# Performance work log

Measured on AMD Instinct MI355X. Metric: run time of the kernel, lower is better.

## Reference

```python
import jax, jax.numpy as jnp
import numpy as np

# Conv config (matches init_kwargs): 3x3 conv, 256->256, stride 1, pad 1
KH, KW = 3, 3
STRIDE = (1, 1)
PAD = ((1, 1), (1, 1))


def setup_inputs() -> dict:
    key = jax.random.key(0)
    k1, k2, k3 = jax.random.split(key, 3)
    x = jax.random.normal(k1, (32, 256, 56, 56), dtype=jnp.float32)
    # linear.weight = conv.weight.view(C_out, C_in*kH*kW) -> [256, 2304]
    weight = jax.random.normal(k2, (256, 256 * KH * KW), dtype=jnp.float32) * 0.02
    bias = jax.random.normal(k3, (256,), dtype=jnp.float32)
    return {"x": x, "weight": weight, "bias": bias}


def reference(x, weight, bias):
    # im2col (same layout/order as F.unfold: feature dim = C * kH * kW, c-major)
    # patches: [N, C*kH*kW, H_out, W_out]
    patches = jax.lax.conv_general_dilated_patches(
        x, filter_shape=(KH, KW), window_strides=STRIDE, padding=PAD
    )
    # dense GEMM over the unfolded feature dim (the nn.Linear)
    y = jnp.einsum("nkhw,ok->nohw", patches, weight)
    y = y + bias[None, :, None, None]
    return y
```

## Files before the change

kernel.cpp:

```cpp
#include <hip/hip_runtime.h>
#include <hip/hip_bf16.h>

typedef short bf16x8 __attribute__((ext_vector_type(8)));
typedef float f32x4  __attribute__((ext_vector_type(4)));

#define HWHW   3136
#define BH     4
#define NROW   6
#define NCOL   58
#define NJJ    (NROW*NCOL)
#define ROWSH  40
#define CHUNK  32
#define NCHUNK 8

__device__ __forceinline__ unsigned short f2bf(float f) {
    unsigned int u = __float_as_uint(f);
    u += 0x7fffu + ((u >> 16) & 1u);
    return (unsigned short)(u >> 16);
}

__global__ void wprep(const float* __restrict__ w, unsigned short* __restrict__ wt) {
    int idx = blockIdx.x * blockDim.x + threadIdx.x;
    int e    = idx & 7;
    int lane = (idx >> 3) & 63;
    int om   = (idx >> 9) & 15;
    int c8   = (idx >> 13) & 7;
    int t    = idx >> 16;
    int o = om * 16 + (lane & 15);
    int c = c8 * 32 + (lane >> 4) * 8 + e;
    wt[idx] = f2bf(w[o * 2304 + c * 9 + t]);
}

__global__ __launch_bounds__(512, 2)
void conv_kernel(const float* __restrict__ x, const unsigned short* __restrict__ wt,
                 const float* __restrict__ bias, float* __restrict__ out) {
    __shared__ short xs[2][NJJ * ROWSH];

    const int hb = blockIdx.x;
    const int n  = blockIdx.y;
    const int h0 = hb * BH;

    const int tid  = threadIdx.x;
    const int lane = tid & 63;
    const int wv   = tid >> 6;
    const int wm   = wv & 3;
    const int ng   = wv >> 2;
    const int g    = lane >> 4;
    const int lcol = lane & 15;

    int bbase[7];
#pragma unroll
    for (int f = 0; f < 7; ++f) {
        int j = ng * 112 + f * 16 + lcol;
        bbase[f] = ((j / 56) * NCOL + (j % 56)) * ROWSH + 8 * g;
    }

    const int cpair = tid >> 5;
    const int col0  = tid & 31;

    const float* xn = x + (size_t)n * 256 * HWHW;

    float sv0[6][2], sv1[6][2];

    f32x4 acc[4][7];
#pragma unroll
    for (int m = 0; m < 4; ++m)
#pragma unroll
        for (int f = 0; f < 7; ++f) acc[m][f] = (f32x4){0.f, 0.f, 0.f, 0.f};

    const unsigned short* wl = wt + (size_t)lane * 8;

    auto stage_load = [&](int c8) {
        const float* xc0 = xn + (size_t)(c8 * CHUNK + 2 * cpair) * HWHW;
        const float* xc1 = xc0 + HWHW;
#pragma unroll
        for (int r = 0; r < 6; ++r) {
            int hh = h0 - 1 + r;
            bool rok = (hh >= 0) & (hh < 56);
#pragma unroll
            for (int ci = 0; ci < 2; ++ci) {
                int col = col0 + 32 * ci;
                int ww  = col - 1;
                bool ok = rok & (col < 58) & (ww >= 0) & (ww < 56);
                int off = hh * 56 + ww;
                sv0[r][ci] = ok ? xc0[off] : 0.0f;
                sv1[r][ci] = ok ? xc1[off] : 0.0f;
            }
        }
    };
    auto stage_write = [&](int buf) {
#pragma unroll
        for (int r = 0; r < 6; ++r)
#pragma unroll
            for (int ci = 0; ci < 2; ++ci) {
                int col = col0 + 32 * ci;
                if (col < 58) {
                    unsigned int p = (unsigned int)f2bf(sv0[r][ci]) |
                                     ((unsigned int)f2bf(sv1[r][ci]) << 16);
                    *(unsigned int*)&xs[buf][(r * NCOL + col) * ROWSH + 2 * cpair] = p;
                }
            }
    };

    stage_load(0);
    stage_write(0);
    __syncthreads();

    for (int c8 = 0; c8 < NCHUNK; ++c8) {
        if (c8 < NCHUNK - 1) stage_load(c8 + 1);
        const short* xb = &xs[c8 & 1][0];

        bf16x8 a0[4], a1[4];
#pragma unroll
        for (int m = 0; m < 4; ++m)
            a0[m] = *(const bf16x8*)(wl + (size_t)(((0 * 8 + c8) * 16) + 4 * wm + m) * 512);

#pragma unroll
        for (int t = 0; t < 9; ++t) {
            bf16x8* ac = (t & 1) ? a1 : a0;
            bf16x8* an = (t & 1) ? a0 : a1;
            if (t < 8) {
#pragma unroll
                for (int m = 0; m < 4; ++m)
                    an[m] = *(const bf16x8*)(wl + (size_t)((((t + 1) * 8 + c8) * 16) + 4 * wm + m) * 512);
            }
            const int dt = ((t / 3) * NCOL + (t % 3)) * ROWSH;
#pragma unroll
            for (int f = 0; f < 7; ++f) {
                bf16x8 b = *(const bf16x8*)&xb[bbase[f] + dt];
#pragma unroll
                for (int m = 0; m < 4; ++m)
                    acc[m][f] = __builtin_amdgcn_mfma_f32_16x16x32_bf16(ac[m], b, acc[m][f], 0, 0, 0);
            }
        }

        if (c8 < NCHUNK - 1) stage_write((c8 + 1) & 1);
        __syncthreads();
    }

#pragma unroll
    for (int m = 0; m < 4; ++m) {
#pragma unroll
        for (int q = 0; q < 4; ++q) {
            int o = 64 * wm + 16 * m + 4 * g + q;
            float bs = bias[o];
            float* yo = out + ((size_t)n * 256 + o) * HWHW + h0 * 56;
#pragma unroll
            for (int f = 0; f < 7; ++f) {
                int j = ng * 112 + f * 16 + lcol;
                yo[j] = acc[m][f][q] + bs;
            }
        }
    }
}

extern "C" void kernel_launch(void* const* d_in, const int* in_sizes, int n_in,
                              void* d_out, int out_size, void* d_ws, size_t ws_size,
                              hipStream_t stream) {
    const float* x    = (const float*)d_in[0];
    const float* w    = (const float*)d_in[1];
    const float* bias = (const float*)d_in[2];
    float* out        = (float*)d_out;
    unsigned short* wt = (unsigned short*)d_ws;

    wprep<<<2304, 256, 0, stream>>>(w, wt);
    dim3 grid(14, 32);
    conv_kernel<<<grid, 512, 0, stream>>>(x, wt, bias, out);
}
```

Measured before the change: 128.2 us.

## Pre-pad input to bf16 buffer and split output channels across blocks

Adds an xprep kernel that converts the fp32 input into a zero-padded bf16 buffer of shape [N,C,58,64], so the conv kernel can fill shared memory with vector loads instead of bounds-checked scalar fp32 loads. The main conv kernel now runs 256-thread blocks, each covering half the output channels, which doubles the grid. The next chunk's stage loads and writes are interleaved partway through the tap loop, and weight loads are no longer double-buffered in registers. The cost is an extra kernel with a full read and write of the activation, and each input tile is now staged twice, once per channel half. The old kernel is kept as a fallback for when the workspace is too small.

After: 284.0 us. +121.6%, slower.

```diff
diff --git a/kernel.cpp b/kernel.cpp
--- a/kernel.cpp
+++ b/kernel.cpp
@@ -5,13 +5,10 @@
 typedef float f32x4  __attribute__((ext_vector_type(4)));
 
 #define HWHW   3136
-#define BH     4
-#define NROW   6
-#define NCOL   58
-#define NJJ    (NROW*NCOL)
-#define ROWSH  40
-#define CHUNK  32
-#define NCHUNK 8
+#define XP_H   58
+#define XP_W   64
+#define ROWSH  34
+#define NJJ    (6*64)
 
 __device__ __forceinline__ unsigned short f2bf(float f) {
     unsigned int u = __float_as_uint(f);
@@ -31,47 +28,155 @@
     wt[idx] = f2bf(w[o * 2304 + c * 9 + t]);
 }
 
-__global__ __launch_bounds__(512, 2)
-void conv_kernel(const float* __restrict__ x, const unsigned short* __restrict__ wt,
-                 const float* __restrict__ bias, float* __restrict__ out) {
+__global__ void xprep(const float* __restrict__ x, unsigned short* __restrict__ xp) {
+    int idx = blockIdx.x * 256 + threadIdx.x;
+    int n  = blockIdx.y;
+    int q  = idx & 15;
+    int t2 = idx >> 4;
+    int hp = t2 % 58;
+    int c  = t2 / 58;
+    int h_ok = (hp >= 1) & (hp <= 56);
+    const float* xr = x + ((size_t)n * 256 + c) * HWHW + (h_ok ? (hp - 1) : 0) * 56;
+    unsigned int v01 = 0, v23 = 0;
+#pragma unroll
+    for (int e = 0; e < 4; ++e) {
+        int w = q * 4 + e - 1;
+        bool ok = h_ok & (w >= 0) & (w < 56);
+        float f = xr[ok ? w : 0];
+        f = ok ? f : 0.0f;
+        unsigned int b = f2bf(f);
+        if (e < 2) v01 |= b << (16 * e);
+        else       v23 |= b << (16 * (e - 2));
+    }
+    unsigned int* dst = (unsigned int*)(xp + ((((size_t)n * 256 + c) * XP_H) + hp) * XP_W + q * 4);
+    dst[0] = v01;
+    dst[1] = v23;
+}
+
+__global__ __launch_bounds__(256, 2)
+void conv_main(const unsigned short* __restrict__ xp, const unsigned short* __restrict__ wt,
+               const float* __restrict__ bias, float* __restrict__ out) {
     __shared__ short xs[2][NJJ * ROWSH];
 
-    const int hb = blockIdx.x;
+    const int bx = blockIdx.x;
+    const int hb = bx >> 1;
+    const int bm = bx & 1;
     const int n  = blockIdx.y;
-    const int h0 = hb * BH;
+    const int h0 = hb * 4;
 
     const int tid  = threadIdx.x;
     const int lane = tid & 63;
     const int wv   = tid >> 6;
-    const int wm   = wv & 3;
-    const int ng   = wv >> 2;
+    const int wm   = wv & 1;
+    const int ng   = wv >> 1;
     const int g    = lane >> 4;
     const int lcol = lane & 15;
 
-    int bbase[7];
+    int bboff[7];
 #pragma unroll
     for (int f = 0; f < 7; ++f) {
         int j = ng * 112 + f * 16 + lcol;
-        bbase[f] = ((j / 56) * NCOL + (j % 56)) * ROWSH + 8 * g;
-    }
-
-    const int cpair = tid >> 5;
-    const int col0  = tid & 31;
-
+        bboff[f] = (((j / 56) * 64 + (j % 56)) * ROWSH + 8 * g) * 2;
+    }
+
+    const int so = tid & 7;
+    const int sc = (tid >> 3) & 31;
+    const unsigned short* xpt = xp + (((size_t)n * 256 + sc) * XP_H + h0) * XP_W + so * 8;
+    const int swb = ((so * 8) * ROWSH + sc) * 2;
+
+    const unsigned short* wl = wt + (size_t)lane * 8;
+    const int obase = bm * 8 + wm * 4;
+
+    f32x4 acc[4][7];
+#pragma unroll
+    for (int m = 0; m < 4; ++m)
+#pragma unroll
+        for (int f = 0; f < 7; ++f) acc[m][f] = (f32x4){0.f, 0.f, 0.f, 0.f};
+
+    bf16x8 sv[3];
+    auto s_load = [&](int c8, int half) {
+        const unsigned short* p = xpt + (size_t)c8 * 32 * XP_H * XP_W + half * 3 * XP_W;
+#pragma unroll
+        for (int r = 0; r < 3; ++r) sv[r] = *(const bf16x8*)(p + r * XP_W);
+    };
+    auto s_write = [&](int buf, int half) {
+        char* d = (char*)&xs[buf][0] + swb + half * 3 * 64 * ROWSH * 2;
+#pragma unroll
+        for (int r = 0; r < 3; ++r)
+#pragma unroll
+            for (int k = 0; k < 8; ++k)
+                *(short*)(d + r * 64 * ROWSH * 2 + k * ROWSH * 2) = sv[r][k];
+    };
+
+    s_load(0, 0); s_write(0, 0);
+    s_load(0, 1); s_write(0, 1);
+    __syncthreads();
+
+    for (int c8 = 0; c8 < 8; ++c8) {
+        const char* xb = (const char*)&xs[c8 & 1][0];
+        const bool more = c8 < 7;
+        if (more) s_load(c8 + 1, 0);
+
+#pragma unroll
+        for (int t = 0; t < 9; ++t) {
+            bf16x8 a[4];
+#pragma unroll
+            for (int m = 0; m < 4; ++m)
+                a[m] = *(const bf16x8*)(wl + (size_t)((t * 8 + c8) * 16 + obase + m) * 512);
+            const int dt = ((t / 3) * 64 + (t % 3)) * ROWSH * 2;
+#pragma unroll
+            for (int f = 0; f < 7; ++f) {
+                bf16x8 b = *(const bf16x8*)(xb + bboff[f] + dt);
+#pragma unroll
+                for (int m = 0; m < 4; ++m)
+                    acc[m][f] = __builtin_amdgcn_mfma_f32_16x16x32_bf16(a[m], b, acc[m][f], 0, 0, 0);
+            }
+            if (t == 2 && more) { s_write((c8 + 1) & 1, 0); s_load(c8 + 1, 1); }
+            if (t == 5 && more) { s_write((c8 + 1) & 1, 1); }
+        }
+        __syncthreads();
+    }
+
+#pragma unroll
+    for (int m = 0; m < 4; ++m) {
+#pragma unroll
+        for (int q = 0; q < 4; ++q) {
+            int o = bm * 128 + wm * 64 + m * 16 + 4 * g + q;
+            float bs = bias[o];
+            float* yo = out + ((size_t)n * 256 + o) * HWHW + hb * 224;
+#pragma unroll
+            for (int f = 0; f < 7; ++f) {
+                int j = ng * 112 + f * 16 + lcol;
+                yo[j] = acc[m][f][q] + bs;
+            }
+        }
+    }
+}
+
+__global__ __launch_bounds__(512, 2)
+void conv_fallback(const float* __restrict__ x, const unsigned short* __restrict__ wt,
+                   const float* __restrict__ bias, float* __restrict__ out) {
+    __shared__ short xs[2][348 * 40];
+    const int hb = blockIdx.x, n = blockIdx.y, h0 = hb * 4;
+    const int tid = threadIdx.x, lane = tid & 63, wv = tid >> 6;
+    const int wm = wv & 3, ng = wv >> 2, g = lane >> 4, lcol = lane & 15;
+    int bbase[7];
+#pragma unroll
+    for (int f = 0; f < 7; ++f) {
+        int j = ng * 112 + f * 16 + lcol;
+        bbase[f] = ((j / 56) * 58 + (j % 56)) * 40 + 8 * g;
+    }
+    const int cpair = tid >> 5, col0 = tid & 31;
     const float* xn = x + (size_t)n * 256 * HWHW;
-
     float sv0[6][2], sv1[6][2];
-
     f32x4 acc[4][7];
 #pragma unroll
     for (int m = 0; m < 4; ++m)
 #pragma unroll
         for (int f = 0; f < 7; ++f) acc[m][f] = (f32x4){0.f, 0.f, 0.f, 0.f};
-
     const unsigned short* wl = wt + (size_t)lane * 8;
-
     auto stage_load = [&](int c8) {
-        const float* xc0 = xn + (size_t)(c8 * CHUNK + 2 * cpair) * HWHW;
+        const float* xc0 = xn + (size_t)(c8 * 32 + 2 * cpair) * HWHW;
         const float* xc1 = xc0 + HWHW;
 #pragma unroll
         for (int r = 0; r < 6; ++r) {
@@ -79,8 +184,7 @@
             bool rok = (hh >= 0) & (hh < 56);
 #pragma unroll
             for (int ci = 0; ci < 2; ++ci) {
-                int col = col0 + 32 * ci;
-                int ww  = col - 1;
+                int col = col0 + 32 * ci, ww = col - 1;
                 bool ok = rok & (col < 58) & (ww >= 0) & (ww < 56);
                 int off = hh * 56 + ww;
                 sv0[r][ci] = ok ? xc0[off] : 0.0f;
@@ -97,24 +201,19 @@
                 if (col < 58) {
                     unsigned int p = (unsigned int)f2bf(sv0[r][ci]) |
                                      ((unsigned int)f2bf(sv1[r][ci]) << 16);
-                    *(unsigned int*)&xs[buf][(r * NCOL + col) * ROWSH + 2 * cpair] = p;
+                    *(unsigned int*)&xs[buf][(r * 58 + col) * 40 + 2 * cpair] = p;
                 }
             }
     };
-
-    stage_load(0);
-    stage_write(0);
+    stage_load(0); stage_write(0);
     __syncthreads();
-
-    for (int c8 = 0; c8 < NCHUNK; ++c8) {
-        if (c8 < NCHUNK - 1) stage_load(c8 + 1);
+    for (int c8 = 0; c8 < 8; ++c8) {
+        if (c8 < 7) stage_load(c8 + 1);
         const short* xb = &xs[c8 & 1][0];
-
         bf16x8 a0[4], a1[4];
 #pragma unroll
         for (int m = 0; m < 4; ++m)
-            a0[m] = *(const bf16x8*)(wl + (size_t)(((0 * 8 + c8) * 16) + 4 * wm + m) * 512);
-
+            a0[m] = *(const bf16x8*)(wl + (size_t)((c8 * 16) + 4 * wm + m) * 512);
 #pragma unroll
         for (int t = 0; t < 9; ++t) {
             bf16x8* ac = (t & 1) ? a1 : a0;
@@ -124,7 +223,7 @@
                 for (int m = 0; m < 4; ++m)
                     an[m] = *(const bf16x8*)(wl + (size_t)((((t + 1) * 8 + c8) * 16) + 4 * wm + m) * 512);
             }
-            const int dt = ((t / 3) * NCOL + (t % 3)) * ROWSH;
+            const int dt = ((t / 3) * 58 + (t % 3)) * 40;
 #pragma unroll
             for (int f = 0; f < 7; ++f) {
                 bf16x8 b = *(const bf16x8*)&xb[bbase[f] + dt];
@@ -133,11 +232,9 @@
                     acc[m][f] = __builtin_amdgcn_mfma_f32_16x16x32_bf16(ac[m], b, acc[m][f], 0, 0, 0);
             }
         }
-
-        if (c8 < NCHUNK - 1) stage_write((c8 + 1) & 1);
+        if (c8 < 7) stage_write((c8 + 1) & 1);
         __syncthreads();
     }
-
 #pragma unroll
     for (int m = 0; m < 4; ++m) {
 #pragma unroll
@@ -162,8 +259,13 @@
     const float* bias = (const float*)d_in[2];
     float* out        = (float*)d_out;
     unsigned short* wt = (unsigned short*)d_ws;
+    unsigned short* xpad = (unsigned short*)((char*)d_ws + 1179648);
 
     wprep<<<2304, 256, 0, stream>>>(w, wt);
-    dim3 grid(14, 32);
-    conv_kernel<<<grid, 512, 0, stream>>>(x, wt, bias, out);
-}
+    if (ws_size >= (size_t)1179648 + 60817408) {
+        xprep<<<dim3(928, 32), 256, 0, stream>>>(x, xpad);
+        conv_main<<<dim3(28, 32), 256, 0, stream>>>(xpad, wt, bias, out);
+    } else {
+        conv_fallback<<<dim3(14, 32), 512, 0, stream>>>(x, wt, bias, out);
+    }
+}
```
